# Performance work log

Measured on AMD Instinct MI355X. Metric: run time of the kernel, lower is better.

The kernel has to match this reference:

```python
import jax, jax.numpy as jnp
import numpy as np

B, T, D, H, F = 8, 1024, 512, 8, 2048
DK = D // H
EPS = 1e-3  # Keras LayerNormalization default epsilon
NEG = -1e9


def layer_norm(x, g, b):
    mu = jnp.mean(x, axis=-1, keepdims=True)
    var = jnp.mean(jnp.square(x - mu), axis=-1, keepdims=True)
    return (x - mu) * jax.lax.rsqrt(var + EPS) * g + b


def setup_inputs() -> dict:
    key = jax.random.key(0)
    ks = jax.random.split(key, 16)
    s = 1.0 / np.sqrt(D)
    sf = 1.0 / np.sqrt(F)
    x = jax.random.normal(ks[0], (B, T, D), dtype=jnp.float32)
    # binary attention mask (1 = attend). Random block-sparse-ish pattern.
    mask = (jax.random.uniform(ks[1], (B, 1, T, T)) > 0.15).astype(jnp.float32)
    return {
        "x": x,
        "mask": mask,
        "ln_in_g": jnp.ones((D,), jnp.float32),
        "ln_in_b": jnp.zeros((D,), jnp.float32),
        "Wq": jax.random.normal(ks[2], (D, D), jnp.float32) * s,
        "bq": jnp.zeros((D,), jnp.float32),
        "Wk": jax.random.normal(ks[3], (D, D), jnp.float32) * s,
        "bk": jnp.zeros((D,), jnp.float32),
        "Wv": jax.random.normal(ks[4], (D, D), jnp.float32) * s,
        "bv": jnp.zeros((D,), jnp.float32),
        "ln1_g": jnp.ones((D,), jnp.float32),
        "ln1_b": jnp.zeros((D,), jnp.float32),
        "W1": jax.random.normal(ks[5], (D, F), jnp.float32) * s,
        "b1": jnp.zeros((F,), jnp.float32),
        "W2": jax.random.normal(ks[6], (F, D), jnp.float32) * sf,
        "b2": jnp.zeros((D,), jnp.float32),
        "ln2_g": jnp.ones((D,), jnp.float32),
        "ln2_b": jnp.zeros((D,), jnp.float32),
    }


def reference(x, mask, ln_in_g, ln_in_b, Wq, bq, Wk, bk, Wv, bv,
              ln1_g, ln1_b, W1, b1, W2, b2, ln2_g, ln2_b):
    bs = x.shape[0]
    h = layer_norm(x, ln_in_g, ln_in_b)                      # [B,T,D]
    # QKV projections, split heads -> [B,H,T,DK]
    q = (h @ Wq + bq).reshape(bs, -1, H, DK).transpose(0, 2, 1, 3)
    k = (h @ Wk + bk).reshape(bs, -1, H, DK).transpose(0, 2, 1, 3)
    v = (h @ Wv + bv).reshape(bs, -1, H, DK).transpose(0, 2, 1, 3)
    scores = jnp.einsum('bhtd,bhsd->bhts', q, k) / np.sqrt(DK)
    scores = scores + NEG * (1.0 - mask)                     # additive mask
    probs = jax.nn.softmax(scores, axis=-1)                  # dropout: identity at inference
    attn = jnp.einsum('bhts,bhsd->bhtd', probs, v)
    attn = attn.transpose(0, 2, 1, 3).reshape(bs, -1, H * DK)
    # residual with ORIGINAL inputs (pre-ln_in), as in call() -> attend(inputs,...)
    attn = attn + x
    a = layer_norm(attn, ln1_g, ln1_b)
    f = jax.nn.relu(a @ W1 + b1) @ W2 + b2
    out = layer_norm(f + a, ln2_g, ln2_b)
    return out
```

## Files before the change

kernel.cpp:

```cpp
#include <hip/hip_runtime.h>

typedef unsigned short u16;
typedef unsigned long long u64;
typedef __bf16 bf16x8 __attribute__((ext_vector_type(8)));
typedef float f32x4 __attribute__((ext_vector_type(4)));

#define B_ 8
#define T_ 1024
#define D_ 512
#define H_ 8
#define DK_ 64
#define F_ 2048

__device__ __forceinline__ u16 f2bf(float f) {
    unsigned u = __float_as_uint(f);
    u += 0x7fffu + ((u >> 16) & 1u);
    return (u16)(u >> 16);
}

__device__ __forceinline__ void tile_transcvt(
    const float* __restrict__ W, u16* __restrict__ WT, int K, int N, int k0, int n0,
    u16 (*t)[72])
{
    const int tid = threadIdx.x;
    const int r = tid >> 2, c4 = (tid & 3) * 16;
    const float* src = W + (size_t)(k0 + r) * N + n0 + c4;
#pragma unroll
    for (int j = 0; j < 16; j += 4) {
        float4 v = *(const float4*)(src + j);
        t[r][c4 + j]     = f2bf(v.x);
        t[r][c4 + j + 1] = f2bf(v.y);
        t[r][c4 + j + 2] = f2bf(v.z);
        t[r][c4 + j + 3] = f2bf(v.w);
    }
    __syncthreads();
    u16 tmp[16];
#pragma unroll
    for (int j = 0; j < 16; ++j) tmp[j] = t[c4 + j][r];
    u16* dst = WT + (size_t)(n0 + r) * K + k0 + c4;
    *(uint4*)dst       = *(uint4*)&tmp[0];
    *(uint4*)(dst + 8) = *(uint4*)&tmp[8];
}

__global__ __launch_bounds__(256) void prep_all(
    const float* __restrict__ Wq, const float* __restrict__ Wk, const float* __restrict__ Wv,
    const float* __restrict__ bq, const float* __restrict__ bk, const float* __restrict__ bv,
    const float* __restrict__ W1, const float* __restrict__ W2,
    const float* __restrict__ mask,
    u16* __restrict__ WqkvT, u16* __restrict__ W1T, u16* __restrict__ W2T,
    float* __restrict__ bias, u64* __restrict__ Mb)
{
    __shared__ u16 t[64][72];
    const int blk = blockIdx.x;
    const int tid = threadIdx.x;
    if (blk < 192) {
        const int k0 = (blk & 7) * 64;
        const int n0 = (blk >> 3) * 64;
        const float* W = (n0 < 512) ? Wq : (n0 < 1024 ? Wk : Wv);
        if (k0 == 0 && tid < 64) {
            int n = n0 + tid;
            bias[n] = (n < 512) ? bq[n] : (n < 1024 ? bk[n - 512] : bv[n - 1024]);
        }
        const int r = tid >> 2, c4 = (tid & 3) * 16;
        const float* src = W + (size_t)(k0 + r) * 512 + (n0 & 511) + c4;
#pragma unroll
        for (int j = 0; j < 16; j += 4) {
            float4 v = *(const float4*)(src + j);
            t[r][c4 + j]     = f2bf(v.x);
            t[r][c4 + j + 1] = f2bf(v.y);
            t[r][c4 + j + 2] = f2bf(v.z);
            t[r][c4 + j + 3] = f2bf(v.w);
        }
        __syncthreads();
        u16 tmp[16];
#pragma unroll
        for (int j = 0; j < 16; ++j) tmp[j] = t[c4 + j][r];
        u16* dst = WqkvT + (size_t)(n0 + r) * 512 + k0 + c4;
        *(uint4*)dst       = *(uint4*)&tmp[0];
        *(uint4*)(dst + 8) = *(uint4*)&tmp[8];
    } else if (blk < 448) {
        const int idx = blk - 192;
        tile_transcvt(W1, W1T, 512, 2048, (idx & 7) * 64, (idx >> 3) * 64, t);
    } else if (blk < 704) {
        const int idx = blk - 448;
        tile_transcvt(W2, W2T, 2048, 512, (idx & 31) * 64, (idx >> 5) * 64, t);
    } else {
        const int idx = blk - 704;
        int gw = (idx * 256 + tid) >> 6;
        int lane = tid & 63;
#pragma unroll
        for (int i = 0; i < 16; ++i) {
            size_t chunk = (size_t)gw * 16 + i;
            float v = mask[chunk * 64 + lane];
            u64 bm = __ballot(v > 0.5f);
            if (lane == 0) Mb[chunk] = bm;
        }
    }
}

__global__ __launch_bounds__(256) void ln_kernel(
    const float* __restrict__ X, const float* __restrict__ R,
    const float* __restrict__ g, const float* __restrict__ bt,
    u16* __restrict__ ob, float* __restrict__ of)
{
    int wave = threadIdx.x >> 6, lane = threadIdx.x & 63;
    int row = blockIdx.x * 4 + wave;
    size_t base = (size_t)row * D_ + lane * 8;
    float v[8];
    float4 a0 = *(const float4*)(X + base);
    float4 a1 = *(const float4*)(X + base + 4);
    v[0]=a0.x; v[1]=a0.y; v[2]=a0.z; v[3]=a0.w;
    v[4]=a1.x; v[5]=a1.y; v[6]=a1.z; v[7]=a1.w;
    if (R) {
        float4 r0 = *(const float4*)(R + base);
        float4 r1 = *(const float4*)(R + base + 4);
        v[0]+=r0.x; v[1]+=r0.y; v[2]+=r0.z; v[3]+=r0.w;
        v[4]+=r1.x; v[5]+=r1.y; v[6]+=r1.z; v[7]+=r1.w;
    }
    float s = 0.f, q = 0.f;
#pragma unroll
    for (int j = 0; j < 8; ++j) { s += v[j]; q += v[j] * v[j]; }
#pragma unroll
    for (int off = 32; off > 0; off >>= 1) {
        s += __shfl_xor(s, off);
        q += __shfl_xor(q, off);
    }
    float mu = s * (1.0f / D_);
    float var = q * (1.0f / D_) - mu * mu;
    float rstd = rsqrtf(var + 1e-3f);
    int c0 = lane * 8;
    float y[8];
#pragma unroll
    for (int j = 0; j < 8; ++j) y[j] = (v[j] - mu) * rstd * g[c0 + j] + bt[c0 + j];
    if (ob) {
        u16 t[8];
#pragma unroll
        for (int j = 0; j < 8; ++j) t[j] = f2bf(y[j]);
        *(uint4*)(ob + base) = *(uint4*)t;
    }
    if (of) {
        float4 o0, o1;
        o0.x=y[0]; o0.y=y[1]; o0.z=y[2]; o0.w=y[3];
        o1.x=y[4]; o1.y=y[5]; o1.z=y[6]; o1.w=y[7];
        *(float4*)(of + base) = o0;
        *(float4*)(of + base + 4) = o1;
    }
}

template<int BN, int RELU, int OUTBF, int WRITE_VT>
__global__ __launch_bounds__(256) void gemm_db(
    const u16* __restrict__ A, const u16* __restrict__ BT,
    const float* __restrict__ bias, u16* __restrict__ Cb,
    float* __restrict__ Cf, u16* __restrict__ Vt, int M, int N, int K)
{
    constexpr int NI = BN / 32;
    __shared__ u16 As[2][128 * 32];
    __shared__ u16 Bs[2][BN * 32];
    const int tid = threadIdx.x;
    const int wave = tid >> 6, lane = tid & 63;
    const int quad = lane >> 4, l16 = lane & 15;
    const int wr = wave >> 1, wc = wave & 1;
    const int rowBase = blockIdx.y * 128;
    const int colBase = blockIdx.x * BN;
    const int lr = lane >> 2;
    const int lc = (lane & 3) * 8;
    const u16* Abase = A  + (size_t)(rowBase + lr) * K + lc;
    const u16* Bbase = BT + (size_t)(colBase + lr) * K + lc;

    auto stage = [&](int k0, int buf) {
#pragma unroll
        for (int c = 0; c < 2; ++c) {
            int chunk = wave * 2 + c;
            const u16* gp = Abase + (size_t)(chunk * 16) * K + k0;
            __builtin_amdgcn_global_load_lds(
                (const __attribute__((address_space(1))) unsigned int*)gp,
                (__attribute__((address_space(3))) unsigned int*)&As[buf][chunk * 512],
                16, 0, 0);
        }
#pragma unroll
        for (int c = 0; c < BN / 64; ++c) {
            int chunk = wave * (BN / 64) + c;
            const u16* gp = Bbase + (size_t)(chunk * 16) * K + k0;
            __builtin_amdgcn_global_load_lds(
                (const __attribute__((address_space(1))) unsigned int*)gp,
                (__attribute__((address_space(3))) unsigned int*)&Bs[buf][chunk * 512],
                16, 0, 0);
        }
    };

    f32x4 acc[4][NI] = {};
    stage(0, 0);
    for (int k0 = 0; k0 < K; k0 += 32) {
        const int buf = (k0 >> 5) & 1;
        __syncthreads();
        if (k0 + 32 < K) stage(k0 + 32, buf ^ 1);
        bf16x8 af[4], bfr[NI];
#pragma unroll
        for (int i = 0; i < 4; ++i)
            af[i] = *(const bf16x8*)&As[buf][(wr * 64 + i * 16 + l16) * 32 + quad * 8];
#pragma unroll
        for (int j = 0; j < NI; ++j)
            bfr[j] = *(const bf16x8*)&Bs[buf][(wc * (BN / 2) + j * 16 + l16) * 32 + quad * 8];
#pragma unroll
        for (int i = 0; i < 4; ++i)
#pragma unroll
            for (int j = 0; j < NI; ++j)
                acc[i][j] = __builtin_amdgcn_mfma_f32_16x16x32_bf16(af[i], bfr[j], acc[i][j], 0, 0, 0);
    }
#pragma unroll
    for (int i = 0; i < 4; ++i) {
        int row0 = rowBase + wr * 64 + i * 16 + quad * 4;
#pragma unroll
        for (int j = 0; j < NI; ++j) {
            int col = colBase + wc * (BN / 2) + j * 16 + l16;
            float bv = bias[col];
#pragma unroll
            for (int r = 0; r < 4; ++r) {
                float v = acc[i][j][r] + bv;
                if (RELU) v = fmaxf(v, 0.0f);
                if (WRITE_VT && col >= 1024) {
                    int hv = col - 1024;
                    int row = row0 + r;
                    Vt[((size_t)((row >> 10) * 8 + (hv >> 6)) * 64 + (hv & 63)) * T_ + (row & 1023)] = f2bf(v);
                } else if (OUTBF) {
                    Cb[(size_t)(row0 + r) * N + col] = f2bf(v);
                } else {
                    Cf[(size_t)(row0 + r) * N + col] = v;
                }
            }
        }
    }
}

__global__ __launch_bounds__(256) void attn_kernel(
    const u16* __restrict__ QKV, const u16* __restrict__ Vt,
    const u64* __restrict__ Mb, float* __restrict__ Out)
{
    const int flat = blockIdx.x + 16 * (blockIdx.y + 8 * blockIdx.z);
    const int xcd = flat & 7, slot = flat >> 3;
    const int bh = xcd * 8 + (slot >> 4);
    const int qt = slot & 15;
    const int b = bh >> 3, h = bh & 7;
    const int qBase = qt * 64;
    const int tid = threadIdx.x;
    const int wave = tid >> 6, lane = tid & 63;
    const int quad = lane >> 4, l16 = lane & 15;
    __shared__ u16 Ks[64][72];
    __shared__ u16 Vs[64][72];
    __shared__ u16 Ps[4][16][72];

    const int qRow = qBase + wave * 16 + l16;
    const u16* qptr = QKV + ((size_t)(b * T_) + qRow) * (3 * D_) + h * DK_;
    bf16x8 qf0 = *(const bf16x8*)(qptr + quad * 8);
    bf16x8 qf1 = *(const bf16x8*)(qptr + 32 + quad * 8);

    float l_i[4] = {0.f, 0.f, 0.f, 0.f};
    f32x4 o[4] = {{0,0,0,0},{0,0,0,0},{0,0,0,0},{0,0,0,0}};

    const int sr = tid >> 2;
    const int sc = (tid & 3) * 8;
    const u16* Kg = QKV + (size_t)(b * T_) * (3 * D_) + D_ + h * DK_;
    const u16* Vg = Vt + (size_t)(b * H_ + h) * DK_ * T_;
    const u64* Mg = Mb + ((size_t)(b * T_) + qBase + wave * 16 + quad * 4) * (T_ / 64);

    uint4 kb0 = *(const uint4*)(Kg + (size_t)sr * (3 * D_) + sc);
    uint4 kb1 = *(const uint4*)(Kg + (size_t)sr * (3 * D_) + sc + 32);
    uint4 vb0 = *(const uint4*)(Vg + (size_t)sr * T_ + sc);
    uint4 vb1 = *(const uint4*)(Vg + (size_t)sr * T_ + sc + 32);

    for (int s0 = 0; s0 < T_; s0 += 64) {
        __syncthreads();
        *(uint4*)&Ks[sr][sc]      = kb0;
        *(uint4*)&Ks[sr][sc + 32] = kb1;
        *(uint4*)&Vs[sr][sc]      = vb0;
        *(uint4*)&Vs[sr][sc + 32] = vb1;
        __syncthreads();
        if (s0 + 64 < T_) {
            int s1 = s0 + 64;
            kb0 = *(const uint4*)(Kg + (size_t)(s1 + sr) * (3 * D_) + sc);
            kb1 = *(const uint4*)(Kg + (size_t)(s1 + sr) * (3 * D_) + sc + 32);
            vb0 = *(const uint4*)(Vg + (size_t)sr * T_ + s1 + sc);
            vb1 = *(const uint4*)(Vg + (size_t)sr * T_ + s1 + sc + 32);
        }

        u64 m64[4];
#pragma unroll
        for (int r = 0; r < 4; ++r) m64[r] = Mg[(size_t)r * (T_ / 64) + (s0 >> 6)];

#pragma unroll
        for (int n = 0; n < 4; ++n) {
            f32x4 s4 = {0.f, 0.f, 0.f, 0.f};
            bf16x8 kf0 = *(const bf16x8*)&Ks[n * 16 + l16][quad * 8];
            bf16x8 kf1 = *(const bf16x8*)&Ks[n * 16 + l16][32 + quad * 8];
            s4 = __builtin_amdgcn_mfma_f32_16x16x32_bf16(qf0, kf0, s4, 0, 0, 0);
            s4 = __builtin_amdgcn_mfma_f32_16x16x32_bf16(qf1, kf1, s4, 0, 0, 0);
#pragma unroll
            for (int r = 0; r < 4; ++r) {
                float p = __expf(fmaf(s4[r], 0.125f, -10.0f));
                p = ((m64[r] >> (n * 16 + l16)) & 1ull) ? p : 0.0f;
                l_i[r] += p;
                Ps[wave][quad * 4 + r][n * 16 + l16] = f2bf(p);
            }
        }
        bf16x8 pf0 = *(const bf16x8*)&Ps[wave][l16][quad * 8];
        bf16x8 pf1 = *(const bf16x8*)&Ps[wave][l16][32 + quad * 8];
#pragma unroll
        for (int dt = 0; dt < 4; ++dt) {
            bf16x8 vf0 = *(const bf16x8*)&Vs[dt * 16 + l16][quad * 8];
            bf16x8 vf1 = *(const bf16x8*)&Vs[dt * 16 + l16][32 + quad * 8];
            o[dt] = __builtin_amdgcn_mfma_f32_16x16x32_bf16(pf0, vf0, o[dt], 0, 0, 0);
            o[dt] = __builtin_amdgcn_mfma_f32_16x16x32_bf16(pf1, vf1, o[dt], 0, 0, 0);
        }
    }
#pragma unroll
    for (int off = 1; off < 16; off <<= 1) {
#pragma unroll
        for (int r = 0; r < 4; ++r) l_i[r] += __shfl_xor(l_i[r], off);
    }
    float inv[4];
#pragma unroll
    for (int r = 0; r < 4; ++r) inv[r] = 1.0f / l_i[r];
    const int orow = qBase + wave * 16 + quad * 4;
    float* Ob = Out + ((size_t)(b * T_) + orow) * D_ + h * DK_;
#pragma unroll
    for (int dt = 0; dt < 4; ++dt) {
#pragma unroll
        for (int r = 0; r < 4; ++r)
            Ob[(size_t)r * D_ + dt * 16 + l16] = o[dt][r] * inv[r];
    }
}

extern "C" void kernel_launch(void* const* d_in, const int* in_sizes, int n_in,
                              void* d_out, int out_size, void* d_ws, size_t ws_size,
                              hipStream_t stream)
{
    const float* x       = (const float*)d_in[0];
    const float* mask    = (const float*)d_in[1];
    const float* ln_in_g = (const float*)d_in[2];
    const float* ln_in_b = (const float*)d_in[3];
    const float* Wq      = (const float*)d_in[4];
    const float* bq      = (const float*)d_in[5];
    const float* Wk      = (const float*)d_in[6];
    const float* bk      = (const float*)d_in[7];
    const float* Wv      = (const float*)d_in[8];
    const float* bv      = (const float*)d_in[9];
    const float* ln1_g   = (const float*)d_in[10];
    const float* ln1_b   = (const float*)d_in[11];
    const float* W1      = (const float*)d_in[12];
    const float* b1      = (const float*)d_in[13];
    const float* W2      = (const float*)d_in[14];
    const float* b2      = (const float*)d_in[15];
    const float* ln2_g   = (const float*)d_in[16];
    const float* ln2_b   = (const float*)d_in[17];
    float* out = (float*)d_out;

    char* ws = (char*)d_ws;
    size_t off = 0;
    auto alloc = [&](size_t bytes) -> void* {
        void* p = ws + off;
        off = (off + bytes + 255) & ~(size_t)255;
        return p;
    };
    u16*   WqkvT   = (u16*)alloc((size_t)1536 * 512 * 2);
    u16*   W1T     = (u16*)alloc((size_t)2048 * 512 * 2);
    u16*   W2T     = (u16*)alloc((size_t)512 * 2048 * 2);
    float* bias_q  = (float*)alloc(1536 * 4);
    u64*   Mb      = (u64*)alloc((size_t)B_ * T_ * (T_ / 64) * 8);
    u16*   h_bf    = (u16*)alloc((size_t)8192 * 512 * 2);
    u16*   QKV     = (u16*)alloc((size_t)8192 * 1536 * 2);
    u16*   Vt      = (u16*)alloc((size_t)B_ * H_ * DK_ * T_ * 2);
    float* attn    = (float*)alloc((size_t)8192 * 512 * 4);
    u16*   a_bf    = (u16*)alloc((size_t)8192 * 512 * 2);
    float* a_f     = (float*)alloc((size_t)8192 * 512 * 4);
    u16*   f1      = (u16*)alloc((size_t)8192 * 2048 * 2);
    float* f2      = (float*)alloc((size_t)8192 * 512 * 4);
    if (off > ws_size) return;

    prep_all<<<2752, 256, 0, stream>>>(Wq, Wk, Wv, bq, bk, bv, W1, W2, mask,
                                       WqkvT, W1T, W2T, bias_q, Mb);

    ln_kernel<<<2048, 256, 0, stream>>>(x, nullptr, ln_in_g, ln_in_b, h_bf, nullptr);

    gemm_db<128, 0, 1, 1><<<dim3(1536 / 128, 8192 / 128), 256, 0, stream>>>(
        h_bf, WqkvT, bias_q, QKV, nullptr, Vt, 8192, 1536, 512);

    attn_kernel<<<dim3(T_ / 64, H_, B_), 256, 0, stream>>>(QKV, Vt, Mb, attn);

    ln_kernel<<<2048, 256, 0, stream>>>(attn, x, ln1_g, ln1_b, a_bf, a_f);

    gemm_db<128, 1, 1, 0><<<dim3(2048 / 128, 8192 / 128), 256, 0, stream>>>(
        a_bf, W1T, b1, f1, nullptr, nullptr, 8192, 2048, 512);

    gemm_db<64, 0, 0, 0><<<dim3(512 / 64, 8192 / 128), 256, 0, stream>>>(
        f1, W2T, b2, nullptr, f2, nullptr, 8192, 512, 2048);

    ln_kernel<<<2048, 256, 0, stream>>>(f2, a_f, ln2_g, ln2_b, nullptr, out);
}
```

Measured before the change: 301.5 us.

## Move V transpose into separate LDS-tiled kernel, prefetch mask, repad attention LDS

The V-transpose scatter is taken out of the QKV GEMM epilogue, where it issued strided 2-byte global writes, and done in a dedicated kernel that stages 64x64 tiles in LDS and writes coalesced 16-byte rows. The attention kernel now prefetches the next tile's mask words together with the K/V prefetch, and widens LDS row padding from 72 to 88 elements to change the bank-conflict pattern. The extra kernel adds a launch and a read/write pass over V in exchange for cheaper GEMM stores.

```diff
diff --git a/kernel.cpp b/kernel.cpp
--- a/kernel.cpp
+++ b/kernel.cpp
@@ -147,11 +147,11 @@
     }
 }
 
-template<int BN, int RELU, int OUTBF, int WRITE_VT>
+template<int BN, int RELU, int OUTBF>
 __global__ __launch_bounds__(256) void gemm_db(
     const u16* __restrict__ A, const u16* __restrict__ BT,
     const float* __restrict__ bias, u16* __restrict__ Cb,
-    float* __restrict__ Cf, u16* __restrict__ Vt, int M, int N, int K)
+    float* __restrict__ Cf, int M, int N, int K)
 {
     constexpr int NI = BN / 32;
     __shared__ u16 As[2][128 * 32];
@@ -218,20 +218,36 @@
             for (int r = 0; r < 4; ++r) {
                 float v = acc[i][j][r] + bv;
                 if (RELU) v = fmaxf(v, 0.0f);
-                if (WRITE_VT && col >= 1024) {
-                    int hv = col - 1024;
-                    int row = row0 + r;
-                    Vt[((size_t)((row >> 10) * 8 + (hv >> 6)) * 64 + (hv & 63)) * T_ + (row & 1023)] = f2bf(v);
-                } else if (OUTBF) {
-                    Cb[(size_t)(row0 + r) * N + col] = f2bf(v);
-                } else {
-                    Cf[(size_t)(row0 + r) * N + col] = v;
-                }
+                if (OUTBF) Cb[(size_t)(row0 + r) * N + col] = f2bf(v);
+                else       Cf[(size_t)(row0 + r) * N + col] = v;
             }
         }
     }
 }
 
+__global__ __launch_bounds__(256) void vtrans(const u16* __restrict__ QKV, u16* __restrict__ Vt)
+{
+    int blk = blockIdx.x;
+    int bh = blk >> 4;
+    int t0 = (blk & 15) * 64;
+    int b = bh >> 3, h = bh & 7;
+    __shared__ u16 tile[64][72];
+    int tid = threadIdx.x;
+    int r = tid >> 2;
+    int c = (tid & 3) * 16;
+    const u16* src = QKV + ((size_t)(b * T_) + t0 + r) * (3 * D_) + 2 * D_ + h * DK_ + c;
+    *(uint4*)&tile[r][c]     = *(const uint4*)(src);
+    *(uint4*)&tile[r][c + 8] = *(const uint4*)(src + 8);
+    __syncthreads();
+    u16 tmp[16];
+#pragma unroll
+    for (int j = 0; j < 16; ++j) tmp[j] = tile[c + j][r];
+    u16* dst = Vt + ((size_t)bh * DK_ + r) * T_ + t0 + c;
+    *(uint4*)dst       = *(uint4*)&tmp[0];
+    *(uint4*)(dst + 8) = *(uint4*)&tmp[8];
+}
+
+#define APAD 88
 __global__ __launch_bounds__(256) void attn_kernel(
     const u16* __restrict__ QKV, const u16* __restrict__ Vt,
     const u64* __restrict__ Mb, float* __restrict__ Out)
@@ -245,9 +261,9 @@
     const int tid = threadIdx.x;
     const int wave = tid >> 6, lane = tid & 63;
     const int quad = lane >> 4, l16 = lane & 15;
-    __shared__ u16 Ks[64][72];
-    __shared__ u16 Vs[64][72];
-    __shared__ u16 Ps[4][16][72];
+    __shared__ u16 Ks[64][APAD];
+    __shared__ u16 Vs[64][APAD];
+    __shared__ u16 Ps[4][16][APAD];
 
     const int qRow = qBase + wave * 16 + l16;
     const u16* qptr = QKV + ((size_t)(b * T_) + qRow) * (3 * D_) + h * DK_;
@@ -267,6 +283,9 @@
     uint4 kb1 = *(const uint4*)(Kg + (size_t)sr * (3 * D_) + sc + 32);
     uint4 vb0 = *(const uint4*)(Vg + (size_t)sr * T_ + sc);
     uint4 vb1 = *(const uint4*)(Vg + (size_t)sr * T_ + sc + 32);
+    u64 m64[4];
+#pragma unroll
+    for (int r = 0; r < 4; ++r) m64[r] = Mg[(size_t)r * (T_ / 64)];
 
     for (int s0 = 0; s0 < T_; s0 += 64) {
         __syncthreads();
@@ -275,17 +294,18 @@
         *(uint4*)&Vs[sr][sc]      = vb0;
         *(uint4*)&Vs[sr][sc + 32] = vb1;
         __syncthreads();
+        u64 mcur[4];
+#pragma unroll
+        for (int r = 0; r < 4; ++r) mcur[r] = m64[r];
         if (s0 + 64 < T_) {
             int s1 = s0 + 64;
             kb0 = *(const uint4*)(Kg + (size_t)(s1 + sr) * (3 * D_) + sc);
             kb1 = *(const uint4*)(Kg + (size_t)(s1 + sr) * (3 * D_) + sc + 32);
             vb0 = *(const uint4*)(Vg + (size_t)sr * T_ + s1 + sc);
             vb1 = *(const uint4*)(Vg + (size_t)sr * T_ + s1 + sc + 32);
-        }
-
-        u64 m64[4];
-#pragma unroll
-        for (int r = 0; r < 4; ++r) m64[r] = Mg[(size_t)r * (T_ / 64) + (s0 >> 6)];
+#pragma unroll
+            for (int r = 0; r < 4; ++r) m64[r] = Mg[(size_t)r * (T_ / 64) + (s1 >> 6)];
+        }
 
 #pragma unroll
         for (int n = 0; n < 4; ++n) {
@@ -297,7 +317,7 @@
 #pragma unroll
             for (int r = 0; r < 4; ++r) {
                 float p = __expf(fmaf(s4[r], 0.125f, -10.0f));
-                p = ((m64[r] >> (n * 16 + l16)) & 1ull) ? p : 0.0f;
+                p = ((mcur[r] >> (n * 16 + l16)) & 1ull) ? p : 0.0f;
                 l_i[r] += p;
                 Ps[wave][quad * 4 + r][n * 16 + l16] = f2bf(p);
             }
@@ -381,18 +401,20 @@
 
     ln_kernel<<<2048, 256, 0, stream>>>(x, nullptr, ln_in_g, ln_in_b, h_bf, nullptr);
 
-    gemm_db<128, 0, 1, 1><<<dim3(1536 / 128, 8192 / 128), 256, 0, stream>>>(
-        h_bf, WqkvT, bias_q, QKV, nullptr, Vt, 8192, 1536, 512);
+    gemm_db<128, 0, 1><<<dim3(1536 / 128, 8192 / 128), 256, 0, stream>>>(
+        h_bf, WqkvT, bias_q, QKV, nullptr, 8192, 1536, 512);
+
+    vtrans<<<1024, 256, 0, stream>>>(QKV, Vt);
 
     attn_kernel<<<dim3(T_ / 64, H_, B_), 256, 0, stream>>>(QKV, Vt, Mb, attn);
 
     ln_kernel<<<2048, 256, 0, stream>>>(attn, x, ln1_g, ln1_b, a_bf, a_f);
 
-    gemm_db<128, 1, 1, 0><<<dim3(2048 / 128, 8192 / 128), 256, 0, stream>>>(
-        a_bf, W1T, b1, f1, nullptr, nullptr, 8192, 2048, 512);
-
-    gemm_db<64, 0, 0, 0><<<dim3(512 / 64, 8192 / 128), 256, 0, stream>>>(
-        f1, W2T, b2, nullptr, f2, nullptr, 8192, 512, 2048);
+    gemm_db<128, 1, 1><<<dim3(2048 / 128, 8192 / 128), 256, 0, stream>>>(
+        a_bf, W1T, b1, f1, nullptr, 8192, 2048, 512);
+
+    gemm_db<64, 0, 0><<<dim3(512 / 64, 8192 / 128), 256, 0, stream>>>(
+        f1, W2T, b2, nullptr, f2, 8192, 512, 2048);
 
     ln_kernel<<<2048, 256, 0, stream>>>(f2, a_f, ln2_g, ln2_b, nullptr, out);
 }
```

Result: no change. 302.4 us (+0.3%).
